# Performance work log

Measured on AMD Instinct MI355X. Metric: run time of the kernel, lower is better.

Reference implementation:

```python
import jax, jax.numpy as jnp
import numpy as np

N, E, R, G, IN, H, C = 100000, 400000, 4, 64, 64, 128, 2


def setup_inputs() -> dict:
    key = jax.random.key(0)
    ks = jax.random.split(key, 20)
    s = 0.05
    inp = {
        "x": jax.random.normal(ks[0], (N, IN), jnp.float32),
        "src": jax.random.randint(ks[1], (R, E), 0, N, jnp.int32),
        "dst": jax.random.randint(ks[2], (R, E), 0, N, jnp.int32),
        "graph_ids": jnp.sort(jax.random.randint(ks[3], (N,), 0, G, jnp.int32)),
        "W_in": jax.random.normal(ks[4], (IN, H), jnp.float32) * s,
        "b_in": jnp.zeros((H,), jnp.float32),
        "W1": jax.random.normal(ks[5], (R, H, H), jnp.float32) * s,
        "b1": jnp.zeros((R, H), jnp.float32),
        "W2": jax.random.normal(ks[6], (R, H, H), jnp.float32) * s,
        "b2": jnp.zeros((R, H), jnp.float32),
        "Wm1": jax.random.normal(ks[7], (H, H), jnp.float32) * s,
        "bm1": jnp.zeros((H,), jnp.float32),
        "Wm2": jax.random.normal(ks[8], (H, H), jnp.float32) * s,
        "bm2": jnp.zeros((H,), jnp.float32),
        "Wm3": jax.random.normal(ks[9], (H, C), jnp.float32) * s,
        "bm3": jnp.zeros((C,), jnp.float32),
    }
    return inp


def _gconv(x, src, dst, W, b):
    # DGL GraphConv, norm='both': D_in^{-1/2} A^T D_out^{-1/2} x W + b
    ones_e = jnp.ones(src.shape[0], x.dtype)
    deg_out = jnp.maximum(jax.ops.segment_sum(ones_e, src, num_segments=N), 1.0)
    deg_in = jnp.maximum(jax.ops.segment_sum(ones_e, dst, num_segments=N), 1.0)
    m = x * jax.lax.rsqrt(deg_out)[:, None]          # [N,H] normalized source feats
    agg = jax.ops.segment_sum(m[src], dst, num_segments=N)  # scatter-add over edges
    agg = agg * jax.lax.rsqrt(deg_in)[:, None]
    return agg @ W + b


def _hetero_layer(x, src, dst, W, b):
    # HeteroGraphConv with aggregate='sum' over relations
    out = jnp.zeros((N, W.shape[-1]), x.dtype)
    for r in range(R):
        out = out + _gconv(x, src[r], dst[r], W[r], b[r])
    return out


def reference(x, src, dst, graph_ids, W_in, b_in, W1, b1, W2, b2, Wm1, bm1, Wm2, bm2, Wm3, bm3):
    h = jax.nn.relu(x @ W_in + b_in)                 # input_linear + ReLU
    h = jax.nn.relu(_hetero_layer(h, src, dst, W1, b1))  # RGCN conv1 + ReLU
    h = _hetero_layer(h, src, dst, W2, b2)               # RGCN conv2
    # per-graph mean pooling (replaces the Python element loop)
    counts = jnp.maximum(jax.ops.segment_sum(jnp.ones(N, h.dtype), graph_ids, num_segments=G), 1.0)
    pooled = jax.ops.segment_sum(h, graph_ids, num_segments=G) / counts[:, None]
    # MLP head
    z = jax.nn.relu(pooled @ Wm1 + bm1)
    z = jax.nn.relu(z @ Wm2 + bm2)
    return z @ Wm3 + bm3                             # [G, C]
```

## Files before the change

### kernel.cpp

```cpp
#include <hip/hip_runtime.h>

constexpr int kN = 100000;
constexpr int kE = 400000;
constexpr int kR = 4;
constexpr int kG = 64;
constexpr int kIN = 64;
constexpr int kH = 128;
constexpr int kC = 2;

constexpr int SCAN_TPB = 256;
constexpr int SCAN_CHUNK = 1024;
constexpr int NBLK = (kN + SCAN_CHUNK - 1) / SCAN_CHUNK;

constexpr size_t SZ_H  = (size_t)kN * kH * 4;
constexpr size_t SZ_RN = (size_t)kR * kN * 4;
constexpr size_t SZ_RE = (size_t)kR * kE * 4;
constexpr size_t OFF_HA   = 0;
constexpr size_t OFF_HB   = OFF_HA + SZ_H;
constexpr size_t OFF_DEGO = OFF_HB + SZ_H;
constexpr size_t OFF_DEGI = OFF_DEGO + SZ_RN;
constexpr size_t OFF_CUR  = OFF_DEGI + SZ_RN;
constexpr size_t OFF_PRE  = OFF_CUR + SZ_RN;
constexpr size_t OFF_CSRS = OFF_PRE + SZ_RN;
constexpr size_t OFF_CSRC = OFF_CSRS + SZ_RE;
constexpr size_t OFF_BSUM = OFF_CSRC + SZ_RE;
constexpr size_t OFF_POOL = OFF_BSUM + 4096;
constexpr size_t OFF_Z1   = OFF_POOL + (size_t)kG * kH * 4;
constexpr size_t OFF_Z2   = OFF_Z1 + (size_t)kG * kH * 4;
constexpr size_t OFF_WB1  = OFF_Z2 + (size_t)kG * kH * 4;
constexpr size_t OFF_WB2  = OFF_WB1 + (size_t)kH * kR * kH * 2;

typedef __attribute__((ext_vector_type(8))) short bf16x8;
typedef __attribute__((ext_vector_type(4))) float f32x4;

__device__ inline unsigned short f2bf(float f) {
    unsigned u = __builtin_bit_cast(unsigned, f);
    u += 0x7FFFu + ((u >> 16) & 1u);
    return (unsigned short)(u >> 16);
}
__device__ inline float bf2f_lo(unsigned p) {
    unsigned u = p << 16;
    return __builtin_bit_cast(float, u);
}
__device__ inline float bf2f_hi(unsigned p) {
    unsigned u = p & 0xFFFF0000u;
    return __builtin_bit_cast(float, u);
}


__global__ void k_deg(const int* __restrict__ src, const int* __restrict__ dst,
                      int* __restrict__ deg_o, int* __restrict__ deg_i) {
    int i = blockIdx.x * blockDim.x + threadIdx.x;
    if (i >= kR * kE) return;
    int r = i / kE;
    atomicAdd(&deg_o[r * kN + src[i]], 1);
    atomicAdd(&deg_i[r * kN + dst[i]], 1);
}

__global__ void k_scan1(const int* __restrict__ counts, int* __restrict__ prefix,
                        int* __restrict__ bsums) {
    __shared__ int lds[SCAN_TPB];
    int r = blockIdx.x / NBLK;
    int b = blockIdx.x % NBLK;
    int base = b * SCAN_CHUNK;
    int t = threadIdx.x;
    int v[4]; int s = 0;
    #pragma unroll
    for (int k = 0; k < 4; k++) {
        int idx = base + t * 4 + k;
        v[k] = (idx < kN) ? counts[r * kN + idx] : 0;
        s += v[k];
    }
    lds[t] = s; __syncthreads();
    for (int off = 1; off < SCAN_TPB; off <<= 1) {
        int x = (t >= off) ? lds[t - off] : 0;
        __syncthreads();
        lds[t] += x;
        __syncthreads();
    }
    int ex = (t > 0) ? lds[t - 1] : 0;
    int run = ex;
    #pragma unroll
    for (int k = 0; k < 4; k++) {
        int idx = base + t * 4 + k;
        if (idx < kN) prefix[r * kN + idx] = run;
        run += v[k];
    }
    if (t == 0) bsums[blockIdx.x] = lds[SCAN_TPB - 1];
}

__global__ void k_scan2(int* __restrict__ bsums) {
    __shared__ int lds[128];
    int t = threadIdx.x;
    for (int r = 0; r < kR; r++) {
        int v = (t < NBLK) ? bsums[r * NBLK + t] : 0;
        lds[t] = v; __syncthreads();
        for (int off = 1; off < 128; off <<= 1) {
            int x = (t >= off) ? lds[t - off] : 0;
            __syncthreads();
            lds[t] += x;
            __syncthreads();
        }
        int ex = (t > 0) ? lds[t - 1] : 0;
        if (t < NBLK) bsums[r * NBLK + t] = ex;
        __syncthreads();
    }
}

__global__ void k_scan3(int* __restrict__ prefix, const int* __restrict__ bsums) {
    int b = blockIdx.x % NBLK;
    int off = bsums[blockIdx.x];
    int r = blockIdx.x / NBLK;
    int base = b * SCAN_CHUNK + threadIdx.x;
    #pragma unroll
    for (int k = 0; k < 4; k++) {
        int idx = base + k * SCAN_TPB;
        if (idx < kN) prefix[r * kN + idx] += off;
    }
}

__global__ void k_fill(const int* __restrict__ src, const int* __restrict__ dst,
                       const int* __restrict__ deg_o, const int* __restrict__ deg_i,
                       const int* __restrict__ prefix, int* __restrict__ cursor,
                       int* __restrict__ csr_src, float* __restrict__ csr_coef) {
    int i = blockIdx.x * blockDim.x + threadIdx.x;
    if (i >= kR * kE) return;
    int r = i / kE;
    int s = src[i], d = dst[i];
    int pos = prefix[r * kN + d] + atomicAdd(&cursor[r * kN + d], 1);
    float co = rsqrtf((float)max(deg_o[r * kN + s], 1)) *
               rsqrtf((float)max(deg_i[r * kN + d], 1));
    csr_src[r * kE + pos] = s;
    csr_coef[r * kE + pos] = co;
}

__global__ void k_wconv(const float* __restrict__ W, unsigned short* __restrict__ Wbt) {
    int i = blockIdx.x * 256 + threadIdx.x;
    if (i >= kR * kH * kH) return;
    int r = i >> 14; int kk = (i >> 7) & 127; int j = i & 127;
    Wbt[(size_t)j * (kR * kH) + r * kH + kk] = f2bf(W[i]);
}

__global__ __launch_bounds__(256) void k_inlin(const float* __restrict__ x,
                                               const float* __restrict__ W,
                                               const float* __restrict__ b,
                                               unsigned short* __restrict__ h) {
    __shared__ float Ws[64][128];
    __shared__ float xs[64][64];
    int t = threadIdx.x;
    int n0 = blockIdx.x * 64;
    for (int i = t; i < 64 * 128; i += 256) Ws[i >> 7][i & 127] = W[i];
    for (int i = t; i < 64 * 64; i += 256) {
        int rr = i >> 6, cc = i & 63;
        int n = n0 + rr;
        xs[rr][cc] = (n < kN) ? x[(size_t)n * kIN + cc] : 0.f;
    }
    __syncthreads();
    int jg = t & 31, j0 = jg * 4, rg = t >> 5;
    float acc[8][4] = {};
    for (int k = 0; k < 64; k++) {
        float4 wv = *(const float4*)&Ws[k][j0];
        #pragma unroll
        for (int i = 0; i < 8; i++) {
            float av = xs[rg * 8 + i][k];
            acc[i][0] += av * wv.x; acc[i][1] += av * wv.y;
            acc[i][2] += av * wv.z; acc[i][3] += av * wv.w;
        }
    }
    #pragma unroll
    for (int i = 0; i < 8; i++) {
        int n = n0 + rg * 8 + i;
        if (n < kN) {
            ushort4 res;
            res.x = f2bf(fmaxf(acc[i][0] + b[j0 + 0], 0.f));
            res.y = f2bf(fmaxf(acc[i][1] + b[j0 + 1], 0.f));
            res.z = f2bf(fmaxf(acc[i][2] + b[j0 + 2], 0.f));
            res.w = f2bf(fmaxf(acc[i][3] + b[j0 + 3], 0.f));
            *(ushort4*)&h[(size_t)n * kH + j0] = res;
        }
    }
}

__global__ __launch_bounds__(256, 5) void k_layer(
    const unsigned short* __restrict__ hin, const int* __restrict__ csr_src,
    const float* __restrict__ csr_coef, const int* __restrict__ prefix,
    const int* __restrict__ cnt, const unsigned short* __restrict__ Wbt,
    const float* __restrict__ brel, unsigned short* __restrict__ out, int doRelu) {
    __shared__ char Asb[32 * 512 * 2];
    int t = threadIdx.x, wave = t >> 6, lane = t & 63;
    int grp = lane >> 4, li = lane & 15;
    int n0 = blockIdx.x * 32;

    #pragma unroll
    for (int batch = 0; batch < 2; batch++) {
        int ni = wave * 8 + batch * 4 + grp;
        int n = n0 + ni;
        #pragma unroll
        for (int r = 0; r < kR; r++) {
            int beg = prefix[r * kN + n];
            int c = cnt[r * kN + n];
            const int* sp = csr_src + (size_t)r * kE + beg;
            const float* cp = csr_coef + (size_t)r * kE + beg;
            int cm = c;
            cm = max(cm, __shfl_xor(cm, 16));
            cm = max(cm, __shfl_xor(cm, 32));
            float a0 = 0.f, a1 = 0.f, a2 = 0.f, a3 = 0.f;
            float a4 = 0.f, a5 = 0.f, a6 = 0.f, a7 = 0.f;
            for (int e0 = 0; e0 < cm; e0 += 4) {
                int  sv0 = sp[e0+0], sv1 = sp[e0+1], sv2 = sp[e0+2], sv3 = sp[e0+3];
                float w0 = cp[e0+0], w1 = cp[e0+1], w2 = cp[e0+2], w3 = cp[e0+3];
                bool k0 = (e0+0) < c, k1 = (e0+1) < c, k2 = (e0+2) < c, k3 = (e0+3) < c;
                int  i0 = k0 ? sv0 : 0, i1 = k1 ? sv1 : 0, i2 = k2 ? sv2 : 0, i3 = k3 ? sv3 : 0;
                float c0 = k0 ? w0 : 0.f, c1 = k1 ? w1 : 0.f, c2 = k2 ? w2 : 0.f, c3 = k3 ? w3 : 0.f;
                uint4 p0 = *(const uint4*)(hin + (size_t)i0 * kH + li * 8);
                uint4 p1 = *(const uint4*)(hin + (size_t)i1 * kH + li * 8);
                uint4 p2 = *(const uint4*)(hin + (size_t)i2 * kH + li * 8);
                uint4 p3 = *(const uint4*)(hin + (size_t)i3 * kH + li * 8);
                a0 += c0*bf2f_lo(p0.x); a1 += c0*bf2f_hi(p0.x);
                a2 += c0*bf2f_lo(p0.y); a3 += c0*bf2f_hi(p0.y);
                a4 += c0*bf2f_lo(p0.z); a5 += c0*bf2f_hi(p0.z);
                a6 += c0*bf2f_lo(p0.w); a7 += c0*bf2f_hi(p0.w);
                a0 += c1*bf2f_lo(p1.x); a1 += c1*bf2f_hi(p1.x);
                a2 += c1*bf2f_lo(p1.y); a3 += c1*bf2f_hi(p1.y);
                a4 += c1*bf2f_lo(p1.z); a5 += c1*bf2f_hi(p1.z);
                a6 += c1*bf2f_lo(p1.w); a7 += c1*bf2f_hi(p1.w);
                a0 += c2*bf2f_lo(p2.x); a1 += c2*bf2f_hi(p2.x);
                a2 += c2*bf2f_lo(p2.y); a3 += c2*bf2f_hi(p2.y);
                a4 += c2*bf2f_lo(p2.z); a5 += c2*bf2f_hi(p2.z);
                a6 += c2*bf2f_lo(p2.w); a7 += c2*bf2f_hi(p2.w);
                a0 += c3*bf2f_lo(p3.x); a1 += c3*bf2f_hi(p3.x);
                a2 += c3*bf2f_lo(p3.y); a3 += c3*bf2f_hi(p3.y);
                a4 += c3*bf2f_lo(p3.z); a5 += c3*bf2f_hi(p3.z);
                a6 += c3*bf2f_lo(p3.w); a7 += c3*bf2f_hi(p3.w);
            }
            uint4 pk;
            pk.x = (unsigned)f2bf(a0) | ((unsigned)f2bf(a1) << 16);
            pk.y = (unsigned)f2bf(a2) | ((unsigned)f2bf(a3) << 16);
            pk.z = (unsigned)f2bf(a4) | ((unsigned)f2bf(a5) << 16);
            pk.w = (unsigned)f2bf(a6) | ((unsigned)f2bf(a7) << 16);
            int byte = ni * 1024 + ((r * 256 + li * 16) ^ ((ni & 7) << 4));
            *(uint4*)(Asb + byte) = pk;
        }
    }
    __syncthreads();

    int colA = lane & 15;
    int kgrp = lane >> 4;
    f32x4 acc00 = {}, acc01 = {}, acc10 = {}, acc11 = {};
    const unsigned short* Wb0 = Wbt + (size_t)(wave * 32 + colA) * 512;
    const unsigned short* Wb1 = Wbt + (size_t)(wave * 32 + 16 + colA) * 512;
    int rowA0 = colA, rowA1 = 16 + colA;
    int abase0 = rowA0 * 1024, abase1 = rowA1 * 1024;
    int asw0 = (rowA0 & 7) << 4, asw1 = (rowA1 & 7) << 4;
    for (int kb = 0; kb < 16; kb++) {
        int kbyte = kb * 64 + kgrp * 16;
        bf16x8 af0 = *(const bf16x8*)(Asb + abase0 + (kbyte ^ asw0));
        bf16x8 af1 = *(const bf16x8*)(Asb + abase1 + (kbyte ^ asw1));
        int koff = kb * 32 + kgrp * 8;
        bf16x8 bf0 = *(const bf16x8*)(Wb0 + koff);
        bf16x8 bf1 = *(const bf16x8*)(Wb1 + koff);
        acc00 = __builtin_amdgcn_mfma_f32_16x16x32_bf16(af0, bf0, acc00, 0, 0, 0);
        acc01 = __builtin_amdgcn_mfma_f32_16x16x32_bf16(af0, bf1, acc01, 0, 0, 0);
        acc10 = __builtin_amdgcn_mfma_f32_16x16x32_bf16(af1, bf0, acc10, 0, 0, 0);
        acc11 = __builtin_amdgcn_mfma_f32_16x16x32_bf16(af1, bf1, acc11, 0, 0, 0);
    }
    int col0 = wave * 32 + colA;
    int col1 = wave * 32 + 16 + colA;
    float bias0 = brel[col0] + brel[128 + col0] + brel[256 + col0] + brel[384 + col0];
    float bias1 = brel[col1] + brel[128 + col1] + brel[256 + col1] + brel[384 + col1];
    #pragma unroll
    for (int j = 0; j < 4; j++) {
        int nA = n0 + kgrp * 4 + j;
        int nB = n0 + 16 + kgrp * 4 + j;
        float v00 = acc00[j] + bias0, v01 = acc01[j] + bias1;
        float v10 = acc10[j] + bias0, v11 = acc11[j] + bias1;
        if (doRelu) {
            v00 = fmaxf(v00, 0.f); v01 = fmaxf(v01, 0.f);
            v10 = fmaxf(v10, 0.f); v11 = fmaxf(v11, 0.f);
        }
        out[(size_t)nA * kH + col0] = f2bf(v00);
        out[(size_t)nA * kH + col1] = f2bf(v01);
        out[(size_t)nB * kH + col0] = f2bf(v10);
        out[(size_t)nB * kH + col1] = f2bf(v11);
    }
}

__global__ void k_pool_acc(const unsigned short* __restrict__ h,
                           const int* __restrict__ gid,
                           float* __restrict__ pooled) {
    int j = threadIdx.x;
    int base = blockIdx.x * 128;
    if (base >= kN) return;
    int end = min(base + 128, kN);
    int curg = gid[base];
    float acc = 0.f;
    for (int n = base; n < end; n++) {
        int g = gid[n];
        if (g != curg) {
            atomicAdd(&pooled[curg * kH + j], acc);
            acc = 0.f; curg = g;
        }
        unsigned short v = h[(size_t)n * kH + j];
        acc += __builtin_bit_cast(float, (unsigned)v << 16);
    }
    atomicAdd(&pooled[curg * kH + j], acc);
}

__global__ void k_pool_fin(const int* __restrict__ gid, float* __restrict__ pooled) {
    int g = blockIdx.x, j = threadIdx.x;
    int lo = 0, hi = kN;
    while (lo < hi) { int m = (lo + hi) >> 1; if (gid[m] < g) lo = m + 1; else hi = m; }
    int s = lo;
    lo = s; hi = kN;
    while (lo < hi) { int m = (lo + hi) >> 1; if (gid[m] <= g) lo = m + 1; else hi = m; }
    int c = lo - s;
    pooled[g * kH + j] /= (float)max(c, 1);
}

__global__ void k_head(const float* __restrict__ in, const float* __restrict__ W,
                       const float* __restrict__ b, float* __restrict__ outv, int doRelu) {
    __shared__ float ps[128];
    int g = blockIdx.x, j = threadIdx.x;
    ps[j] = in[g * kH + j];
    __syncthreads();
    float acc = b[j];
    for (int k = 0; k < kH; k++) acc += ps[k] * W[k * kH + j];
    outv[g * kH + j] = doRelu ? fmaxf(acc, 0.f) : acc;
}

__global__ void k_head3(const float* __restrict__ z, const float* __restrict__ W,
                        const float* __restrict__ b, float* __restrict__ outv) {
    int t = threadIdx.x;
    int g = t >> 1, c = t & 1;
    float acc = b[c];
    for (int k = 0; k < kH; k++) acc += z[g * kH + k] * W[k * kC + c];
    outv[g * kC + c] = acc;
}

extern "C" void kernel_launch(void* const* d_in, const int* in_sizes, int n_in,
                              void* d_out, int out_size, void* d_ws, size_t ws_size,
                              hipStream_t stream) {
    (void)in_sizes; (void)n_in; (void)out_size; (void)ws_size;
    const float* x    = (const float*)d_in[0];
    const int*   src  = (const int*)d_in[1];
    const int*   dst  = (const int*)d_in[2];
    const int*   gid  = (const int*)d_in[3];
    const float* W_in = (const float*)d_in[4];
    const float* b_in = (const float*)d_in[5];
    const float* W1   = (const float*)d_in[6];
    const float* b1   = (const float*)d_in[7];
    const float* W2   = (const float*)d_in[8];
    const float* b2   = (const float*)d_in[9];
    const float* Wm1  = (const float*)d_in[10];
    const float* bm1  = (const float*)d_in[11];
    const float* Wm2  = (const float*)d_in[12];
    const float* bm2  = (const float*)d_in[13];
    const float* Wm3  = (const float*)d_in[14];
    const float* bm3  = (const float*)d_in[15];
    float* out = (float*)d_out;

    char* ws = (char*)d_ws;
    unsigned short* h_a = (unsigned short*)(ws + OFF_HA);
    unsigned short* h_b = (unsigned short*)(ws + OFF_HB);
    int*   deg_o   = (int*)(ws + OFF_DEGO);
    int*   deg_i   = (int*)(ws + OFF_DEGI);
    int*   cursor  = (int*)(ws + OFF_CUR);
    int*   prefix  = (int*)(ws + OFF_PRE);
    int*   csr_src = (int*)(ws + OFF_CSRS);
    float* csr_cof = (float*)(ws + OFF_CSRC);
    int*   bsums   = (int*)(ws + OFF_BSUM);
    float* pooled  = (float*)(ws + OFF_POOL);
    float* z1      = (float*)(ws + OFF_Z1);
    float* z2      = (float*)(ws + OFF_Z2);
    unsigned short* wb1 = (unsigned short*)(ws + OFF_WB1);
    unsigned short* wb2 = (unsigned short*)(ws + OFF_WB2);

    hipMemsetAsync(ws + OFF_DEGO, 0, 3 * SZ_RN, stream);
    hipMemsetAsync(ws + OFF_POOL, 0, (size_t)kG * kH * 4, stream);

    int egrid = (kR * kE + 255) / 256;
    k_deg<<<egrid, 256, 0, stream>>>(src, dst, deg_o, deg_i);
    k_scan1<<<kR * NBLK, SCAN_TPB, 0, stream>>>(deg_i, prefix, bsums);
    k_scan2<<<1, 128, 0, stream>>>(bsums);
    k_scan3<<<kR * NBLK, SCAN_TPB, 0, stream>>>(prefix, bsums);
    k_fill<<<egrid, 256, 0, stream>>>(src, dst, deg_o, deg_i, prefix, cursor, csr_src, csr_cof);

    k_wconv<<<(kR * kH * kH + 255) / 256, 256, 0, stream>>>(W1, wb1);
    k_wconv<<<(kR * kH * kH + 255) / 256, 256, 0, stream>>>(W2, wb2);

    k_inlin<<<(kN + 63) / 64, 256, 0, stream>>>(x, W_in, b_in, h_a);

    k_layer<<<kN / 32, 256, 0, stream>>>(h_a, csr_src, csr_cof, prefix, deg_i,
                                         wb1, b1, h_b, 1);
    k_layer<<<kN / 32, 256, 0, stream>>>(h_b, csr_src, csr_cof, prefix, deg_i,
                                         wb2, b2, h_a, 0);

    k_pool_acc<<<(kN + 127) / 128, 128, 0, stream>>>(h_a, gid, pooled);
    k_pool_fin<<<kG, 128, 0, stream>>>(gid, pooled);
    k_head<<<kG, 128, 0, stream>>>(pooled, Wm1, bm1, z1, 1);
    k_head<<<kG, 128, 0, stream>>>(z1, Wm2, bm2, z2, 1);
    k_head3<<<1, 128, 0, stream>>>(z2, Wm3, bm3, out);
}
```

Measured before the change: 649.2 us.

## Pack CSR edges as int2, precompute rsqrt degrees, drop cursor, fuse pool finalize

CSR source index and coefficient are interleaved into one int2 array so each edge needs a single load. The fill step now bumps the prefix array atomically instead of a separate cursor buffer, which removes one memset and one array. Degree rsqrt values are precomputed once in a small kernel, and the destination-side factor is applied per node after aggregation. The gather loop is unrolled to eight edges with the batch loop kept rolled to hold register pressure down, and the pooling-count division is folded into the first head kernel.

```diff
diff --git a/kernel.cpp b/kernel.cpp
--- a/kernel.cpp
+++ b/kernel.cpp
@@ -19,11 +19,11 @@
 constexpr size_t OFF_HB   = OFF_HA + SZ_H;
 constexpr size_t OFF_DEGO = OFF_HB + SZ_H;
 constexpr size_t OFF_DEGI = OFF_DEGO + SZ_RN;
-constexpr size_t OFF_CUR  = OFF_DEGI + SZ_RN;
-constexpr size_t OFF_PRE  = OFF_CUR + SZ_RN;
-constexpr size_t OFF_CSRS = OFF_PRE + SZ_RN;
-constexpr size_t OFF_CSRC = OFF_CSRS + SZ_RE;
-constexpr size_t OFF_BSUM = OFF_CSRC + SZ_RE;
+constexpr size_t OFF_PRE  = OFF_DEGI + SZ_RN;
+constexpr size_t OFF_RSO  = OFF_PRE + SZ_RN;
+constexpr size_t OFF_RSI  = OFF_RSO + SZ_RN;
+constexpr size_t OFF_CSR  = OFF_RSI + SZ_RN;
+constexpr size_t OFF_BSUM = OFF_CSR + 2 * SZ_RE;
 constexpr size_t OFF_POOL = OFF_BSUM + 4096;
 constexpr size_t OFF_Z1   = OFF_POOL + (size_t)kG * kH * 4;
 constexpr size_t OFF_Z2   = OFF_Z1 + (size_t)kG * kH * 4;
@@ -55,6 +55,12 @@
     int r = i / kE;
     atomicAdd(&deg_o[r * kN + src[i]], 1);
     atomicAdd(&deg_i[r * kN + dst[i]], 1);
+}
+
+__global__ void k_rs(const int* __restrict__ deg, float* __restrict__ rs) {
+    int i = blockIdx.x * blockDim.x + threadIdx.x;
+    if (i >= 2 * kR * kN) return;
+    rs[i] = rsqrtf((float)max(deg[i], 1));
 }
 
 __global__ void k_scan1(const int* __restrict__ counts, int* __restrict__ prefix,
@@ -120,18 +126,15 @@
 }
 
 __global__ void k_fill(const int* __restrict__ src, const int* __restrict__ dst,
-                       const int* __restrict__ deg_o, const int* __restrict__ deg_i,
-                       const int* __restrict__ prefix, int* __restrict__ cursor,
-                       int* __restrict__ csr_src, float* __restrict__ csr_coef) {
+                       const float* __restrict__ rs_o, int* __restrict__ prefix,
+                       int2* __restrict__ csr) {
     int i = blockIdx.x * blockDim.x + threadIdx.x;
     if (i >= kR * kE) return;
     int r = i / kE;
     int s = src[i], d = dst[i];
-    int pos = prefix[r * kN + d] + atomicAdd(&cursor[r * kN + d], 1);
-    float co = rsqrtf((float)max(deg_o[r * kN + s], 1)) *
-               rsqrtf((float)max(deg_i[r * kN + d], 1));
-    csr_src[r * kE + pos] = s;
-    csr_coef[r * kE + pos] = co;
+    int pos = atomicAdd(&prefix[r * kN + d], 1);
+    float co = rs_o[r * kN + s];
+    csr[(size_t)r * kE + pos] = make_int2(s, __builtin_bit_cast(int, co));
 }
 
 __global__ void k_wconv(const float* __restrict__ W, unsigned short* __restrict__ Wbt) {
@@ -182,57 +185,54 @@
 }
 
 __global__ __launch_bounds__(256, 5) void k_layer(
-    const unsigned short* __restrict__ hin, const int* __restrict__ csr_src,
-    const float* __restrict__ csr_coef, const int* __restrict__ prefix,
-    const int* __restrict__ cnt, const unsigned short* __restrict__ Wbt,
+    const unsigned short* __restrict__ hin, const int2* __restrict__ csr,
+    const int* __restrict__ prefix, const int* __restrict__ cnt,
+    const float* __restrict__ rs_i, const unsigned short* __restrict__ Wbt,
     const float* __restrict__ brel, unsigned short* __restrict__ out, int doRelu) {
     __shared__ char Asb[32 * 512 * 2];
     int t = threadIdx.x, wave = t >> 6, lane = t & 63;
     int grp = lane >> 4, li = lane & 15;
     int n0 = blockIdx.x * 32;
 
-    #pragma unroll
+    #pragma unroll 1
     for (int batch = 0; batch < 2; batch++) {
         int ni = wave * 8 + batch * 4 + grp;
         int n = n0 + ni;
         #pragma unroll
         for (int r = 0; r < kR; r++) {
-            int beg = prefix[r * kN + n];
-            int c = cnt[r * kN + n];
-            const int* sp = csr_src + (size_t)r * kE + beg;
-            const float* cp = csr_coef + (size_t)r * kE + beg;
+            int end = prefix[r * kN + n];
+            int c   = cnt[r * kN + n];
+            const int2* ep = csr + (size_t)r * kE + (end - c);
+            float rsi = rs_i[r * kN + n];
             int cm = c;
             cm = max(cm, __shfl_xor(cm, 16));
             cm = max(cm, __shfl_xor(cm, 32));
             float a0 = 0.f, a1 = 0.f, a2 = 0.f, a3 = 0.f;
             float a4 = 0.f, a5 = 0.f, a6 = 0.f, a7 = 0.f;
-            for (int e0 = 0; e0 < cm; e0 += 4) {
-                int  sv0 = sp[e0+0], sv1 = sp[e0+1], sv2 = sp[e0+2], sv3 = sp[e0+3];
-                float w0 = cp[e0+0], w1 = cp[e0+1], w2 = cp[e0+2], w3 = cp[e0+3];
-                bool k0 = (e0+0) < c, k1 = (e0+1) < c, k2 = (e0+2) < c, k3 = (e0+3) < c;
-                int  i0 = k0 ? sv0 : 0, i1 = k1 ? sv1 : 0, i2 = k2 ? sv2 : 0, i3 = k3 ? sv3 : 0;
-                float c0 = k0 ? w0 : 0.f, c1 = k1 ? w1 : 0.f, c2 = k2 ? w2 : 0.f, c3 = k3 ? w3 : 0.f;
-                uint4 p0 = *(const uint4*)(hin + (size_t)i0 * kH + li * 8);
-                uint4 p1 = *(const uint4*)(hin + (size_t)i1 * kH + li * 8);
-                uint4 p2 = *(const uint4*)(hin + (size_t)i2 * kH + li * 8);
-                uint4 p3 = *(const uint4*)(hin + (size_t)i3 * kH + li * 8);
-                a0 += c0*bf2f_lo(p0.x); a1 += c0*bf2f_hi(p0.x);
-                a2 += c0*bf2f_lo(p0.y); a3 += c0*bf2f_hi(p0.y);
-                a4 += c0*bf2f_lo(p0.z); a5 += c0*bf2f_hi(p0.z);
-                a6 += c0*bf2f_lo(p0.w); a7 += c0*bf2f_hi(p0.w);
-                a0 += c1*bf2f_lo(p1.x); a1 += c1*bf2f_hi(p1.x);
-                a2 += c1*bf2f_lo(p1.y); a3 += c1*bf2f_hi(p1.y);
-                a4 += c1*bf2f_lo(p1.z); a5 += c1*bf2f_hi(p1.z);
-                a6 += c1*bf2f_lo(p1.w); a7 += c1*bf2f_hi(p1.w);
-                a0 += c2*bf2f_lo(p2.x); a1 += c2*bf2f_hi(p2.x);
-                a2 += c2*bf2f_lo(p2.y); a3 += c2*bf2f_hi(p2.y);
-                a4 += c2*bf2f_lo(p2.z); a5 += c2*bf2f_hi(p2.z);
-                a6 += c2*bf2f_lo(p2.w); a7 += c2*bf2f_hi(p2.w);
-                a0 += c3*bf2f_lo(p3.x); a1 += c3*bf2f_hi(p3.x);
-                a2 += c3*bf2f_lo(p3.y); a3 += c3*bf2f_hi(p3.y);
-                a4 += c3*bf2f_lo(p3.z); a5 += c3*bf2f_hi(p3.z);
-                a6 += c3*bf2f_lo(p3.w); a7 += c3*bf2f_hi(p3.w);
+            for (int e0 = 0; e0 < cm; e0 += 8) {
+                int2 ev[8];
+                #pragma unroll
+                for (int u = 0; u < 8; u++) ev[u] = ep[e0 + u];
+                uint4 pv[8];
+                float co[8];
+                #pragma unroll
+                for (int u = 0; u < 8; u++) {
+                    bool k = (e0 + u) < c;
+                    int idx = k ? ev[u].x : 0;
+                    co[u] = k ? __builtin_bit_cast(float, ev[u].y) : 0.f;
+                    pv[u] = *(const uint4*)(hin + (size_t)idx * kH + li * 8);
+                }
+                #pragma unroll
+                for (int u = 0; u < 8; u++) {
+                    float cu = co[u];
+                    a0 += cu * bf2f_lo(pv[u].x); a1 += cu * bf2f_hi(pv[u].x);
+                    a2 += cu * bf2f_lo(pv[u].y); a3 += cu * bf2f_hi(pv[u].y);
+                    a4 += cu * bf2f_lo(pv[u].z); a5 += cu * bf2f_hi(pv[u].z);
+                    a6 += cu * bf2f_lo(pv[u].w); a7 += cu * bf2f_hi(pv[u].w);
+                }
             }
+            a0 *= rsi; a1 *= rsi; a2 *= rsi; a3 *= rsi;
+            a4 *= rsi; a5 *= rsi; a6 *= rsi; a7 *= rsi;
             uint4 pk;
             pk.x = (unsigned)f2bf(a0) | ((unsigned)f2bf(a1) << 16);
             pk.y = (unsigned)f2bf(a2) | ((unsigned)f2bf(a3) << 16);
@@ -306,22 +306,21 @@
     atomicAdd(&pooled[curg * kH + j], acc);
 }
 
-__global__ void k_pool_fin(const int* __restrict__ gid, float* __restrict__ pooled) {
-    int g = blockIdx.x, j = threadIdx.x;
-    int lo = 0, hi = kN;
-    while (lo < hi) { int m = (lo + hi) >> 1; if (gid[m] < g) lo = m + 1; else hi = m; }
-    int s = lo;
-    lo = s; hi = kN;
-    while (lo < hi) { int m = (lo + hi) >> 1; if (gid[m] <= g) lo = m + 1; else hi = m; }
-    int c = lo - s;
-    pooled[g * kH + j] /= (float)max(c, 1);
-}
-
 __global__ void k_head(const float* __restrict__ in, const float* __restrict__ W,
-                       const float* __restrict__ b, float* __restrict__ outv, int doRelu) {
+                       const float* __restrict__ b, float* __restrict__ outv,
+                       int doRelu, const int* __restrict__ gid) {
     __shared__ float ps[128];
     int g = blockIdx.x, j = threadIdx.x;
-    ps[j] = in[g * kH + j];
+    float v = in[g * kH + j];
+    if (gid) {
+        int lo = 0, hi = kN;
+        while (lo < hi) { int m = (lo + hi) >> 1; if (gid[m] < g) lo = m + 1; else hi = m; }
+        int s = lo;
+        lo = s; hi = kN;
+        while (lo < hi) { int m = (lo + hi) >> 1; if (gid[m] <= g) lo = m + 1; else hi = m; }
+        v /= (float)max(lo - s, 1);
+    }
+    ps[j] = v;
     __syncthreads();
     float acc = b[j];
     for (int k = 0; k < kH; k++) acc += ps[k] * W[k * kH + j];
@@ -364,10 +363,10 @@
     unsigned short* h_b = (unsigned short*)(ws + OFF_HB);
     int*   deg_o   = (int*)(ws + OFF_DEGO);
     int*   deg_i   = (int*)(ws + OFF_DEGI);
-    int*   cursor  = (int*)(ws + OFF_CUR);
     int*   prefix  = (int*)(ws + OFF_PRE);
-    int*   csr_src = (int*)(ws + OFF_CSRS);
-    float* csr_cof = (float*)(ws + OFF_CSRC);
+    float* rs_o    = (float*)(ws + OFF_RSO);
+    float* rs_i    = (float*)(ws + OFF_RSI);
+    int2*  csr     = (int2*)(ws + OFF_CSR);
     int*   bsums   = (int*)(ws + OFF_BSUM);
     float* pooled  = (float*)(ws + OFF_POOL);
     float* z1      = (float*)(ws + OFF_Z1);
@@ -375,29 +374,29 @@
     unsigned short* wb1 = (unsigned short*)(ws + OFF_WB1);
     unsigned short* wb2 = (unsigned short*)(ws + OFF_WB2);
 
-    hipMemsetAsync(ws + OFF_DEGO, 0, 3 * SZ_RN, stream);
+    hipMemsetAsync(ws + OFF_DEGO, 0, 2 * SZ_RN, stream);
     hipMemsetAsync(ws + OFF_POOL, 0, (size_t)kG * kH * 4, stream);
 
     int egrid = (kR * kE + 255) / 256;
     k_deg<<<egrid, 256, 0, stream>>>(src, dst, deg_o, deg_i);
+    k_rs<<<(2 * kR * kN + 255) / 256, 256, 0, stream>>>(deg_o, rs_o);
     k_scan1<<<kR * NBLK, SCAN_TPB, 0, stream>>>(deg_i, prefix, bsums);
     k_scan2<<<1, 128, 0, stream>>>(bsums);
     k_scan3<<<kR * NBLK, SCAN_TPB, 0, stream>>>(prefix, bsums);
-    k_fill<<<egrid, 256, 0, stream>>>(src, dst, deg_o, deg_i, prefix, cursor, csr_src, csr_cof);
+    k_fill<<<egrid, 256, 0, stream>>>(src, dst, rs_o, prefix, csr);
 
     k_wconv<<<(kR * kH * kH + 255) / 256, 256, 0, stream>>>(W1, wb1);
     k_wconv<<<(kR * kH * kH + 255) / 256, 256, 0, stream>>>(W2, wb2);
 
     k_inlin<<<(kN + 63) / 64, 256, 0, stream>>>(x, W_in, b_in, h_a);
 
-    k_layer<<<kN / 32, 256, 0, stream>>>(h_a, csr_src, csr_cof, prefix, deg_i,
+    k_layer<<<kN / 32, 256, 0, stream>>>(h_a, csr, prefix, deg_i, rs_i,
                                          wb1, b1, h_b, 1);
-    k_layer<<<kN / 32, 256, 0, stream>>>(h_b, csr_src, csr_cof, prefix, deg_i,
+    k_layer<<<kN / 32, 256, 0, stream>>>(h_b, csr, prefix, deg_i, rs_i,
                                          wb2, b2, h_a, 0);
 
     k_pool_acc<<<(kN + 127) / 128, 128, 0, stream>>>(h_a, gid, pooled);
-    k_pool_fin<<<kG, 128, 0, stream>>>(gid, pooled);
-    k_head<<<kG, 128, 0, stream>>>(pooled, Wm1, bm1, z1, 1);
-    k_head<<<kG, 128, 0, stream>>>(z1, Wm2, bm2, z2, 1);
+    k_head<<<kG, 128, 0, stream>>>(pooled, Wm1, bm1, z1, 1, gid);
+    k_head<<<kG, 128, 0, stream>>>(z1, Wm2, bm2, z2, 1, nullptr);
     k_head3<<<1, 128, 0, stream>>>(z2, Wm3, bm3, out);
 }
```

Result: no change. 647.4 us (-0.3%).
